# Performance work log

Hardware: AMD Instinct MI355X
Metric: run time of the kernel (lower is better)

The kernel has to match this reference:

```python
import jax, jax.numpy as jnp
import numpy as np

N_NODES = 50000
N_HYPEREDGES = 10000
N_INC = 800000  # incidences (edges in the bipartite node-hyperedge graph)
D = 128
NEG_SLOPE = 0.2


def segment_softmax(logits, seg, num_segments):
    # numerically stable softmax within segments (grouped by seg)
    m = jax.ops.segment_max(logits, seg, num_segments=num_segments)
    e = jnp.exp(logits - m[seg])
    s = jax.ops.segment_sum(e, seg, num_segments=num_segments)
    return e / s[seg]


def safe_inv(d):
    return jnp.where(d > 0, 1.0 / d, 0.0)


def setup_inputs() -> dict:
    key = jax.random.key(0)
    ks = jax.random.split(key, 8)
    x = jax.random.normal(ks[0], (N_NODES, D), dtype=jnp.float32)
    idx0 = jax.random.randint(ks[1], (N_INC,), 0, N_NODES)          # node ids
    idx1 = jax.random.randint(ks[2], (N_INC,), 0, N_HYPEREDGES)     # hyperedge ids
    hyperedge_index = jnp.stack([idx0, idx1], axis=0).astype(jnp.int64)
    hyperedge_weight = jnp.ones((N_HYPEREDGES,), dtype=jnp.float32)
    sc = 1.0 / np.sqrt(D)
    W_lin = jax.random.normal(ks[3], (D, D), dtype=jnp.float32) * sc
    W_lin2 = jax.random.normal(ks[4], (D, D), dtype=jnp.float32) * sc
    W_lin3 = jax.random.normal(ks[5], (D, D), dtype=jnp.float32) * sc
    att = jax.random.normal(ks[6], (1, 1, 2 * D), dtype=jnp.float32) * sc
    att2 = jax.random.normal(ks[7], (1, 1, 2 * D), dtype=jnp.float32) * sc
    return {"x": x, "hyperedge_index": hyperedge_index,
            "hyperedge_weight": hyperedge_weight,
            "W_lin": W_lin, "W_lin2": W_lin2, "W_lin3": W_lin3,
            "att": att, "att2": att2}


def reference(x, hyperedge_index, hyperedge_weight, W_lin, W_lin2, W_lin3, att, att2):
    N, M = N_NODES, N_HYPEREDGES
    H, F = 1, D
    idx0 = hyperedge_index[0]  # node side  [E]
    idx1 = hyperedge_index[1]  # hyperedge side [E]

    # Hyperedge(): mean-style aggregation of node features into hyperedges
    ones_e = jnp.ones_like(idx1, dtype=x.dtype)
    Binv = safe_inv(jax.ops.segment_sum(ones_e, idx1, num_segments=M))  # [M]
    he0 = jax.ops.segment_sum(x[idx0], idx1, num_segments=M) * Binv[:, None]  # [M,D]

    # linear projections
    xl = (x @ W_lin).reshape(N, H, F)      # [N,H,F]
    hl = (he0 @ W_lin2).reshape(M, H, F)   # [M,H,F]

    # first attention: node-gathered vs hyperedge-gathered, softmax grouped by node
    x_i = xl[idx0]                          # [E,H,F]
    x_j = hl[idx1]                          # [E,H,F]
    alpha = (jnp.concatenate([x_i, x_j], axis=-1) * att).sum(-1)  # [E,H]
    alpha = jax.nn.leaky_relu(alpha, NEG_SLOPE)
    alpha = segment_softmax(alpha, idx0, N)

    # degree normalizations
    Dinv = safe_inv(jax.ops.segment_sum(hyperedge_weight[idx1], idx0, num_segments=N))  # [N]

    # propagate node -> hyperedge: out_e[e] = sum Binv[e]*alpha*x[node]
    msg1 = Binv[idx1][:, None, None] * alpha[:, :, None] * x_i  # [E,H,F]
    out_e = jax.ops.segment_sum(msg1, idx1, num_segments=M)     # [M,H,F]

    # second attention with lin3-transformed hyperedge features
    he2 = (out_e.reshape(M, H * F) @ W_lin3).reshape(M, H, F)
    x_j2 = he2[idx1]
    alpha2 = (jnp.concatenate([x_i, x_j2], axis=-1) * att2).sum(-1)  # [E,H]
    alpha2 = jax.nn.leaky_relu(alpha2, NEG_SLOPE)
    alpha2 = segment_softmax(alpha2, idx0, N)

    # propagate hyperedge -> node: out_n[n] = sum Dinv[n]*alpha2*out_e[hyperedge]
    msg2 = Dinv[idx0][:, None, None] * alpha2[:, :, None] * out_e[idx1]  # [E,H,F]
    out_n = jax.ops.segment_sum(msg2, idx0, num_segments=N)              # [N,H,F]

    return out_n.reshape(N, H * F)
```

## Files before the change

kernel.cpp:

```cpp
#include <hip/hip_runtime.h>
#include <math.h>

#define DF 128
#define TILE 8192
#define CAPA 8192
#define CAPB 10240
typedef unsigned int uint;
typedef __attribute__((ext_vector_type(8))) short bf16x8;
typedef __attribute__((ext_vector_type(4))) float f32x4;

__device__ __forceinline__ float leaky(float s){ return s > 0.f ? s : 0.2f*s; }

__device__ __forceinline__ uint bfr(float f){
    uint u = __float_as_uint(f);
    return (u + 0x7fffu + ((u >> 16) & 1u)) >> 16;
}
__device__ __forceinline__ uint bf2(float a, float b){ return bfr(a) | (bfr(b) << 16); }
__device__ __forceinline__ float blo(uint v){ return __uint_as_float(v << 16); }
__device__ __forceinline__ float bhi(uint v){ return __uint_as_float(v & 0xffff0000u); }

__device__ __forceinline__ void load_edge(const void* raw, int is64, int E, int e,
                                          int& n, int& m){
    if (is64){
        const long long* p = (const long long*)raw;
        n = (int)p[e]; m = (int)p[(long long)E + e];
    } else {
        const int* p = (const int*)raw;
        n = p[e]; m = p[E + e];
    }
}

__global__ __launch_bounds__(256) void prep(
        const uint* __restrict__ raw, int* __restrict__ flag,
        int* __restrict__ gcurA, int* __restrict__ gcurB,
        const float* __restrict__ W1, const float* __restrict__ W2,
        const float* __restrict__ W3,
        const float* __restrict__ att, const float* __restrict__ att2,
        float* __restrict__ w2a, float* __restrict__ v1,
        float* __restrict__ v2, float* __restrict__ v3,
        uint* __restrict__ W1t, int E)
{
    int t = threadIdx.x;
    int bid = blockIdx.x;
    if (bid == 0){
        __shared__ int cnt;
        gcurA[t] = t*CAPA;
        gcurB[t] = t*CAPB;
        if (t == 0) cnt = 0;
        __syncthreads();
        int nz = 0;
        for (int i = 0; i < 4; i++){
            int w = 2*(t*4 + i) + 1;
            if (w < 2*E) nz += (raw[w] != 0u);
        }
        atomicAdd(&cnt, nz);
        __syncthreads();
        if (t == 0) *flag = (cnt == 0) ? 1 : 0;
    } else if (bid == 1){
        int d = t & 127;
        const float* W = (t < 128) ? W2 : W1;
        const float* a = (t < 128) ? (att + 128) : att;
        float s = 0.f;
        for (int f = 0; f < 128; f++) s += W[d*128 + f]*a[f];
        if (t < 128) w2a[d] = s; else v1[d] = s;
    } else if (bid == 2){
        __shared__ float sw3a[128];
        int d = t & 127;
        const float* W = (t < 128) ? W1 : W3;
        const float* a = (t < 128) ? att2 : (att2 + 128);
        float s = 0.f;
        for (int f = 0; f < 128; f++) s += W[d*128 + f]*a[f];
        if (t < 128) v2[d] = s; else sw3a[d] = s;
        __syncthreads();
        if (t < 128){
            float s2 = 0.f;
            for (int f = 0; f < 128; f++) s2 += W1[t*128 + f]*sw3a[f];
            v3[t] = s2;
        }
    } else {
        int base = (bid - 3)*1024;
        for (int p = base + t; p < base + 1024; p += 256){
            int f = p >> 6, dh = p & 63;
            W1t[p] = bf2(W1[(2*dh)*128 + f], W1[(2*dh + 1)*128 + f]);
        }
    }
}

__global__ __launch_bounds__(512) void bucket_scatter(const void* __restrict__ raw,
        const int* __restrict__ flag, int* __restrict__ gcurA, int* __restrict__ gcurB,
        uint* __restrict__ bktA, uint* __restrict__ bktB, int E){
    __shared__ uint stA[TILE], stB[TILE];
    __shared__ int hA[256], scA[256], cuA[256], bA[256];
    __shared__ int hB[256], scB[256], cuB[256], bB[256];
    int t = threadIdx.x;
    if (t < 256){ hA[t] = 0; hB[t] = 0; }
    __syncthreads();
    int tb = blockIdx.x*TILE;
    int cnt = min(TILE, E - tb);
    int is64 = *flag;
    for (int i = t; i < cnt; i += 512){
        int n, m; load_edge(raw, is64, E, tb + i, n, m);
        atomicAdd(&hA[n >> 8], 1);
        atomicAdd(&hB[m >> 6], 1);
    }
    __syncthreads();
    if (t < 256){ scA[t] = hA[t]; scB[t] = hB[t]; }
    __syncthreads();
    for (int off = 1; off < 256; off <<= 1){
        int vA = 0, vB = 0;
        if (t < 256 && t >= off){ vA = scA[t - off]; vB = scB[t - off]; }
        __syncthreads();
        if (t < 256){ scA[t] += vA; scB[t] += vB; }
        __syncthreads();
    }
    if (t < 256){
        scA[t] -= hA[t]; scB[t] -= hB[t];
        cuA[t] = scA[t]; cuB[t] = scB[t];
        bA[t] = atomicAdd(&gcurA[t], hA[t]);
        bB[t] = atomicAdd(&gcurB[t], hB[t]);
    }
    __syncthreads();
    for (int i = t; i < cnt; i += 512){
        int n, m; load_edge(raw, is64, E, tb + i, n, m);
        int pA = atomicAdd(&cuA[n >> 8], 1);
        stA[pA] = ((uint)n << 14) | (uint)m;
        int pB = atomicAdd(&cuB[m >> 6], 1);
        stB[pB] = ((uint)m << 16) | (uint)n;
    }
    __syncthreads();
    for (int p = t; p < cnt; p += 512){
        uint v = stA[p]; int b = (int)(v >> 22);
        bktA[bA[b] + (p - scA[b])] = v;
        uint w = stB[p]; int c = (int)(w >> 22);
        bktB[bB[c] + (p - scB[c])] = w;
    }
}

__global__ __launch_bounds__(256) void csr_edge(
        const uint* __restrict__ bktB, const int* __restrict__ gcurB,
        int* __restrict__ adj1, int2* __restrict__ rg1,
        const float* __restrict__ px, float* __restrict__ a1h, int M)
{
    __shared__ int h[64], sc[64], cu[64];
    __shared__ float fsum[64];
    int t = threadIdx.x;
    int b = blockIdx.x;
    int sb = b*CAPB;
    int total = gcurB[b] - sb;
    int kb = b << 6;
    if (t < 64){ h[t] = 0; fsum[t] = 0.f; }
    __syncthreads();
    const uint* src = bktB + sb;
    for (int i = t; i < total; i += 256)
        atomicAdd(&h[(int)(src[i] >> 16) - kb], 1);
    __syncthreads();
    if (t < 64) sc[t] = h[t];
    __syncthreads();
    for (int off = 1; off < 64; off <<= 1){
        int v = (t < 64 && t >= off) ? sc[t - off] : 0;
        __syncthreads();
        if (t < 64) sc[t] += v;
        __syncthreads();
    }
    if (t < 64){ sc[t] -= h[t]; cu[t] = sc[t]; }
    __syncthreads();
    for (int i = t; i < total; i += 256){
        uint v = src[i];
        int k = (int)(v >> 16) - kb;
        int pos = atomicAdd(&cu[k], 1);
        int n = (int)(v & 0xFFFFu);
        adj1[sb + pos] = n;
        atomicAdd(&fsum[k], px[n]);
    }
    __syncthreads();
    int key = kb + t;
    if (t < 64 && key < M){
        rg1[key] = make_int2(sb + sc[t], sb + sc[t] + h[t]);
        a1h[key] = (h[t] > 0) ? fsum[t]/(float)h[t] : 0.f;
    }
}

__global__ __launch_bounds__(256) void csr_node(
        const uint* __restrict__ bktA, const int* __restrict__ gcurA,
        int* __restrict__ adj0, int2* __restrict__ rg0,
        const float* __restrict__ a1x, const float* __restrict__ a1h,
        const float* __restrict__ hw, const float* __restrict__ pxl,
        float4* __restrict__ pk1, float* __restrict__ Dinv, int N)
{
    __shared__ int h[256], sc[256], cu[256];
    __shared__ uint sm[CAPA];
    int t = threadIdx.x;
    int b = blockIdx.x;
    int sb = b*CAPA;
    int total = gcurA[b] - sb;
    int kb = b << 8;
    h[t] = 0;
    __syncthreads();
    const uint* src = bktA + sb;
    for (int i = t; i < total; i += 256)
        atomicAdd(&h[(int)(src[i] >> 14) - kb], 1);
    __syncthreads();
    sc[t] = h[t];
    __syncthreads();
    for (int off = 1; off < 256; off <<= 1){
        int v = (t >= off) ? sc[t - off] : 0;
        __syncthreads();
        sc[t] += v;
        __syncthreads();
    }
    sc[t] -= h[t];
    cu[t] = sc[t];
    __syncthreads();
    for (int i = t; i < total; i += 256){
        uint v = src[i];
        int k = (int)(v >> 14) - kb;
        int pos = atomicAdd(&cu[k], 1);
        sm[pos] = v & 0x3FFFu;
    }
    __syncthreads();
    for (int i = t; i < total; i += 256) adj0[sb + i] = (int)sm[i];
    int key = kb + t;
    if (key < N){
        int deg = h[t], beg = sc[t];
        rg0[key] = make_int2(sb + beg, sb + beg + deg);
        float ax = a1x[key];
        float mb = -3.4e38f, wsum = 0.f;
        for (int j = 0; j < deg; j++){
            int m = (int)sm[beg + j];
            mb = fmaxf(mb, a1h[m]);
            wsum += hw[m];
        }
        float mx = leaky(ax + mb);
        float se = 0.f;
        for (int j = 0; j < deg; j++)
            se += expf(leaky(ax + a1h[(int)sm[beg + j]]) - mx);
        pk1[key] = make_float4(ax, mx, (deg > 0) ? 1.f/se : 0.f, pxl[key]);
        Dinv[key] = (wsum > 0.f) ? 1.f/wsum : 0.f;
    }
}

__global__ __launch_bounds__(256) void gemm_mfma(
    const float* __restrict__ X, const uint* __restrict__ W1t,
    const float* __restrict__ w2a, const float* __restrict__ v1,
    const float* __restrict__ v2, const float* __restrict__ v3,
    uint* __restrict__ xlb, float* __restrict__ a1x, float* __restrict__ a2x,
    float* __restrict__ px, float* __restrict__ pxl, int N)
{
    __shared__ uint4 ldsv[3072];
    char* lds = (char*)ldsv;
    int t = threadIdx.x;
    int lane = t & 63, wv = t >> 6;
    int row0 = blockIdx.x*64;

    {
        const uint4* g = (const uint4*)W1t;
        #pragma unroll
        for (int i = 0; i < 8; i++){
            int u = i*256 + t;
            int col = u >> 4;
            uint4 v = g[u];
            *(uint4*)(lds + 16384 + ((u*16) ^ ((col & 7) << 4))) = v;
        }
    }
    {
        int cg = t & 31;
        float4 c_px = ((const float4*)w2a)[cg];
        float4 c_a1 = ((const float4*)v1 )[cg];
        float4 c_a2 = ((const float4*)v2 )[cg];
        float4 c_pl = ((const float4*)v3 )[cg];
        #pragma unroll
        for (int i = 0; i < 8; i++){
            int idx = i*256 + t;
            int rl = idx >> 5;
            int row = row0 + rl;
            float4 xv = make_float4(0.f, 0.f, 0.f, 0.f);
            if (row < N) xv = ((const float4*)X)[(size_t)row*32 + cg];
            uint2 pk; pk.x = bf2(xv.x, xv.y); pk.y = bf2(xv.z, xv.w);
            *(uint2*)(lds + rl*256 + ((cg*8) ^ ((rl & 7) << 4))) = pk;
            float d0 = xv.x*c_px.x + xv.y*c_px.y + xv.z*c_px.z + xv.w*c_px.w;
            float d1 = xv.x*c_a1.x + xv.y*c_a1.y + xv.z*c_a1.z + xv.w*c_a1.w;
            float d2 = xv.x*c_a2.x + xv.y*c_a2.y + xv.z*c_a2.z + xv.w*c_a2.w;
            float d3 = xv.x*c_pl.x + xv.y*c_pl.y + xv.z*c_pl.z + xv.w*c_pl.w;
            #pragma unroll
            for (int off = 16; off > 0; off >>= 1){
                d0 += __shfl_xor(d0, off); d1 += __shfl_xor(d1, off);
                d2 += __shfl_xor(d2, off); d3 += __shfl_xor(d3, off);
            }
            if (cg == 0 && row < N){
                px[row] = d0; a1x[row] = d1; a2x[row] = d2; pxl[row] = d3;
            }
        }
    }
    __syncthreads();

    f32x4 acc[8];
    #pragma unroll
    for (int i = 0; i < 8; i++) acc[i] = (f32x4){0.f, 0.f, 0.f, 0.f};
    int arow = wv*16 + (lane & 15);
    int aswz = (arow & 7) << 4;
    int bswz = (lane & 7) << 4;
    #pragma unroll
    for (int ks = 0; ks < 4; ks++){
        int au16 = ((lane >> 4) + ks*4)*16;
        bf16x8 af = *(const bf16x8*)(lds + arow*256 + (au16 ^ aswz));
        #pragma unroll
        for (int nf = 0; nf < 8; nf++){
            int bcol = nf*16 + (lane & 15);
            bf16x8 bf = *(const bf16x8*)(lds + 16384 + bcol*256 + (au16 ^ bswz));
            acc[nf] = __builtin_amdgcn_mfma_f32_16x16x32_bf16(af, bf, acc[nf], 0, 0, 0);
        }
    }
    __syncthreads();
    #pragma unroll
    for (int nf = 0; nf < 8; nf++){
        #pragma unroll
        for (int reg = 0; reg < 4; reg++){
            int rl = wv*16 + (lane >> 4)*4 + reg;
            int col = nf*16 + (lane & 15);
            *(unsigned short*)(lds + rl*256 + ((col*2) ^ ((rl & 7) << 4))) =
                (unsigned short)bfr(acc[nf][reg]);
        }
    }
    __syncthreads();
    #pragma unroll
    for (int j = 0; j < 4; j++){
        int unit = j*64 + lane;
        int rl = wv*16 + (unit >> 4);
        int uu = unit & 15;
        uint4 v = *(const uint4*)(lds + rl*256 + ((uu*16) ^ ((rl & 7) << 4)));
        int grow = row0 + rl;
        if (grow < N) ((uint4*)xlb)[(size_t)grow*16 + uu] = v;
    }
}

__global__ __launch_bounds__(256) void agg_oute(
    const int2* __restrict__ rg1, const int* __restrict__ adj1,
    const float4* __restrict__ pk1, const float* __restrict__ a1h,
    const uint* __restrict__ xlb, uint* __restrict__ outeb,
    float* __restrict__ a2h, int M)
{
    int m = blockIdx.x*4 + (threadIdx.x >> 6);
    int lane = threadIdx.x & 63;
    if (m >= M) return;
    int2 r = rg1[m];
    int b = r.x, e = r.y, deg = e - b;
    float binv = deg > 0 ? 1.f/(float)deg : 0.f;
    float ah = a1h[m];
    int sub = lane >> 4, cg = lane & 15;
    const uint4* x4p = (const uint4*)xlb;
    float acc[8] = {0,0,0,0,0,0,0,0};
    float sca = 0.f;
    for (int base = b; base < e; base += 64){
        int cnt = min(64, e - base);
        int n = 0; float al = 0.f;
        if (lane < cnt){
            n = adj1[base + lane];
            float4 g = pk1[n];
            al = expf(leaky(g.x + ah) - g.y) * g.z;
            sca += al * g.w;
        }
        int t4 = 0;
        for (; t4 + 8 <= cnt; t4 += 8){
            int   nb0 = __shfl(n,  t4 + sub);
            float ab0 = __shfl(al, t4 + sub);
            int   nb1 = __shfl(n,  t4 + 4 + sub);
            float ab1 = __shfl(al, t4 + 4 + sub);
            uint4 v0 = x4p[(size_t)nb0*16 + cg];
            uint4 v1 = x4p[(size_t)nb1*16 + cg];
            acc[0] += ab0*blo(v0.x); acc[1] += ab0*bhi(v0.x);
            acc[2] += ab0*blo(v0.y); acc[3] += ab0*bhi(v0.y);
            acc[4] += ab0*blo(v0.z); acc[5] += ab0*bhi(v0.z);
            acc[6] += ab0*blo(v0.w); acc[7] += ab0*bhi(v0.w);
            acc[0] += ab1*blo(v1.x); acc[1] += ab1*bhi(v1.x);
            acc[2] += ab1*blo(v1.y); acc[3] += ab1*bhi(v1.y);
            acc[4] += ab1*blo(v1.z); acc[5] += ab1*bhi(v1.z);
            acc[6] += ab1*blo(v1.w); acc[7] += ab1*bhi(v1.w);
        }
        for (; t4 < cnt; t4 += 4){
            int   nb = __shfl(n,  t4 + sub);
            float ab = __shfl(al, t4 + sub);
            uint4 v = x4p[(size_t)nb*16 + cg];
            acc[0] += ab*blo(v.x); acc[1] += ab*bhi(v.x);
            acc[2] += ab*blo(v.y); acc[3] += ab*bhi(v.y);
            acc[4] += ab*blo(v.z); acc[5] += ab*bhi(v.z);
            acc[6] += ab*blo(v.w); acc[7] += ab*bhi(v.w);
        }
    }
    #pragma unroll
    for (int i = 0; i < 8; i++){
        acc[i] += __shfl_xor(acc[i], 32);
        acc[i] += __shfl_xor(acc[i], 16);
    }
    #pragma unroll
    for (int off = 32; off > 0; off >>= 1) sca += __shfl_xor(sca, off);
    if (lane < 16){
        uint4 w;
        w.x = bf2(binv*acc[0], binv*acc[1]);
        w.y = bf2(binv*acc[2], binv*acc[3]);
        w.z = bf2(binv*acc[4], binv*acc[5]);
        w.w = bf2(binv*acc[6], binv*acc[7]);
        ((uint4*)outeb)[(size_t)m*16 + cg] = w;
    }
    if (lane == 0) a2h[m] = binv*sca;
}

__global__ __launch_bounds__(256) void agg_outn(
    const int2* __restrict__ rg0, const int* __restrict__ adj0,
    const float* __restrict__ a2x, const float* __restrict__ a2h,
    const float* __restrict__ Dinv, const uint* __restrict__ outeb,
    float* __restrict__ out, int N)
{
    int n = blockIdx.x*4 + (threadIdx.x >> 6);
    int lane = threadIdx.x & 63;
    if (n >= N) return;
    int2 r = rg0[n];
    int b = r.x, e = r.y;
    float ax = a2x[n];
    float mbv = -3.4e38f;
    for (int j = b + lane; j < e; j += 64) mbv = fmaxf(mbv, a2h[adj0[j]]);
    #pragma unroll
    for (int off = 32; off > 0; off >>= 1) mbv = fmaxf(mbv, __shfl_xor(mbv, off));
    float mx = leaky(ax + mbv);
    int sub = lane >> 4, cg = lane & 15;
    const uint4* o4p = (const uint4*)outeb;
    float acc[8] = {0,0,0,0,0,0,0,0};
    float sa = 0.f;
    for (int base = b; base < e; base += 64){
        int cnt = min(64, e - base);
        int m = 0; float al = 0.f;
        if (lane < cnt){
            m = adj0[base + lane];
            al = expf(leaky(ax + a2h[m]) - mx);
            sa += al;
        }
        int t4 = 0;
        for (; t4 + 8 <= cnt; t4 += 8){
            int   mb0 = __shfl(m,  t4 + sub);
            float ab0 = __shfl(al, t4 + sub);
            int   mb1 = __shfl(m,  t4 + 4 + sub);
            float ab1 = __shfl(al, t4 + 4 + sub);
            uint4 v0 = o4p[(size_t)mb0*16 + cg];
            uint4 v1 = o4p[(size_t)mb1*16 + cg];
            acc[0] += ab0*blo(v0.x); acc[1] += ab0*bhi(v0.x);
            acc[2] += ab0*blo(v0.y); acc[3] += ab0*bhi(v0.y);
            acc[4] += ab0*blo(v0.z); acc[5] += ab0*bhi(v0.z);
            acc[6] += ab0*blo(v0.w); acc[7] += ab0*bhi(v0.w);
            acc[0] += ab1*blo(v1.x); acc[1] += ab1*bhi(v1.x);
            acc[2] += ab1*blo(v1.y); acc[3] += ab1*bhi(v1.y);
            acc[4] += ab1*blo(v1.z); acc[5] += ab1*bhi(v1.z);
            acc[6] += ab1*blo(v1.w); acc[7] += ab1*bhi(v1.w);
        }
        for (; t4 < cnt; t4 += 4){
            int   mb = __shfl(m,  t4 + sub);
            float ab = __shfl(al, t4 + sub);
            uint4 v = o4p[(size_t)mb*16 + cg];
            acc[0] += ab*blo(v.x); acc[1] += ab*bhi(v.x);
            acc[2] += ab*blo(v.y); acc[3] += ab*bhi(v.y);
            acc[4] += ab*blo(v.z); acc[5] += ab*bhi(v.z);
            acc[6] += ab*blo(v.w); acc[7] += ab*bhi(v.w);
        }
    }
    #pragma unroll
    for (int off = 32; off > 0; off >>= 1) sa += __shfl_xor(sa, off);
    #pragma unroll
    for (int i = 0; i < 8; i++){
        acc[i] += __shfl_xor(acc[i], 32);
        acc[i] += __shfl_xor(acc[i], 16);
    }
    float scale = (sa > 0.f) ? Dinv[n]/sa : 0.f;
    if (lane < 16){
        float4 o0 = make_float4(scale*acc[0], scale*acc[1], scale*acc[2], scale*acc[3]);
        float4 o1 = make_float4(scale*acc[4], scale*acc[5], scale*acc[6], scale*acc[7]);
        ((float4*)out)[(size_t)n*32 + cg*2]     = o0;
        ((float4*)out)[(size_t)n*32 + cg*2 + 1] = o1;
    }
}

extern "C" void kernel_launch(void* const* d_in, const int* in_sizes, int n_in,
                              void* d_out, int out_size, void* d_ws, size_t ws_size,
                              hipStream_t stream){
    const float* x    = (const float*)d_in[0];
    const void*  hidx = d_in[1];
    const float* hw   = (const float*)d_in[2];
    const float* W1   = (const float*)d_in[3];
    const float* W2   = (const float*)d_in[4];
    const float* W3   = (const float*)d_in[5];
    const float* att  = (const float*)d_in[6];
    const float* att2 = (const float*)d_in[7];
    float* out = (float*)d_out;

    const int N = in_sizes[0] / DF;
    const int E = in_sizes[1] / 2;
    const int M = in_sizes[2];

    char* ws = (char*)d_ws;
    size_t o = 0;
    auto take = [&](size_t bytes) -> char* {
        char* p = ws + o;
        o += (bytes + 255) & ~(size_t)255;
        return p;
    };
    const int nbA = (N + 255) >> 8;
    const int nbB = (M + 63) >> 6;

    uint*   xlb  = (uint*)  take((size_t)N*64*4);
    uint*   outeb= (uint*)  take((size_t)M*64*4);
    float*  a1x  = (float*) take((size_t)N*4);
    float*  a2x  = (float*) take((size_t)N*4);
    float*  px   = (float*) take((size_t)N*4);
    float*  pxl  = (float*) take((size_t)N*4);
    float*  Dinv = (float*) take((size_t)N*4);
    float*  a1h  = (float*) take((size_t)M*4);
    float*  a2h  = (float*) take((size_t)M*4);
    float4* pk1  = (float4*)take((size_t)N*16);
    float*  w2a  = (float*) take(DF*4);
    float*  v1   = (float*) take(DF*4);
    float*  v2   = (float*) take(DF*4);
    float*  v3   = (float*) take(DF*4);
    uint*   W1t  = (uint*)  take(128*64*4);
    int2*   rg0  = (int2*)  take((size_t)N*8);
    int2*   rg1  = (int2*)  take((size_t)M*8);
    int*    gcurA= (int*)   take(256*4);
    int*    gcurB= (int*)   take(256*4);
    uint*   bktA = (uint*)  take((size_t)nbA*CAPA*4 + TILE*4);
    uint*   bktB = (uint*)  take((size_t)nbB*CAPB*4 + TILE*4);
    int*    adj0 = (int*)   take((size_t)nbA*CAPA*4);
    int*    adj1 = (int*)   take((size_t)nbB*CAPB*4);
    int*    flag = (int*)   take(256);

    prep<<<11, 256, 0, stream>>>((const uint*)hidx, flag, gcurA, gcurB,
                                 W1, W2, W3, att, att2, w2a, v1, v2, v3, W1t, E);
    bucket_scatter<<<(E + TILE - 1)/TILE, 512, 0, stream>>>(hidx, flag,
                                 gcurA, gcurB, bktA, bktB, E);
    gemm_mfma<<<(N + 63)/64, 256, 0, stream>>>(x, W1t, w2a, v1, v2, v3,
                                               xlb, a1x, a2x, px, pxl, N);
    csr_edge<<<nbB, 256, 0, stream>>>(bktB, gcurB, adj1, rg1, px, a1h, M);
    csr_node<<<nbA, 256, 0, stream>>>(bktA, gcurA, adj0, rg0,
                                      a1x, a1h, hw, pxl, pk1, Dinv, N);
    agg_oute<<<(M + 3)/4, 256, 0, stream>>>(rg1, adj1, pk1, a1h, xlb, outeb, a2h, M);
    agg_outn<<<(N + 3)/4, 256, 0, stream>>>(rg0, adj0, a2x, a2h, Dinv, outeb, out, N);
}
```

Measured before the change: 142.1 us.

## Fuse bucket scatter with GEMM and use global max for softmax shift

Merges the edge bucket-scatter and the bf16 MFMA projection GEMM into one launch, with blocks split by block index, so the two independent stages share the machine and one launch is saved. The per-segment max pass for each softmax is replaced by a single global max of the hyperedge logit, kept in an order-preserving encoded atomicMax. That removes a full gather pass over neighbours in csr_node and agg_outn, but it changes the stabilising shift and risks underflow when logits vary widely. The agg_oute gather loop is also unrolled to keep four loads in flight.

```diff
diff --git a/kernel.cpp b/kernel.cpp
--- a/kernel.cpp
+++ b/kernel.cpp
@@ -18,6 +18,14 @@
 __device__ __forceinline__ uint bf2(float a, float b){ return bfr(a) | (bfr(b) << 16); }
 __device__ __forceinline__ float blo(uint v){ return __uint_as_float(v << 16); }
 __device__ __forceinline__ float bhi(uint v){ return __uint_as_float(v & 0xffff0000u); }
+
+__device__ __forceinline__ uint fenc(float f){
+    uint u = __float_as_uint(f);
+    return (u & 0x80000000u) ? ~u : (u | 0x80000000u);
+}
+__device__ __forceinline__ float fdec(uint k){
+    return (k & 0x80000000u) ? __uint_as_float(k ^ 0x80000000u) : __uint_as_float(~k);
+}
 
 __device__ __forceinline__ void load_edge(const void* raw, int is64, int E, int e,
                                           int& n, int& m){
@@ -31,7 +39,7 @@
 }
 
 __global__ __launch_bounds__(256) void prep(
-        const uint* __restrict__ raw, int* __restrict__ flag,
+        const uint* __restrict__ raw, int* __restrict__ ctrl,
         int* __restrict__ gcurA, int* __restrict__ gcurB,
         const float* __restrict__ W1, const float* __restrict__ W2,
         const float* __restrict__ W3,
@@ -46,7 +54,7 @@
         __shared__ int cnt;
         gcurA[t] = t*CAPA;
         gcurB[t] = t*CAPB;
-        if (t == 0) cnt = 0;
+        if (t == 0){ cnt = 0; ctrl[1] = 0; ctrl[2] = 0; }
         __syncthreads();
         int nz = 0;
         for (int i = 0; i < 4; i++){
@@ -55,7 +63,7 @@
         }
         atomicAdd(&cnt, nz);
         __syncthreads();
-        if (t == 0) *flag = (cnt == 0) ? 1 : 0;
+        if (t == 0) ctrl[0] = (cnt == 0) ? 1 : 0;
     } else if (bid == 1){
         int d = t & 127;
         const float* W = (t < 128) ? W2 : W1;
@@ -86,60 +94,158 @@
     }
 }
 
-__global__ __launch_bounds__(512) void bucket_scatter(const void* __restrict__ raw,
-        const int* __restrict__ flag, int* __restrict__ gcurA, int* __restrict__ gcurB,
-        uint* __restrict__ bktA, uint* __restrict__ bktB, int E){
-    __shared__ uint stA[TILE], stB[TILE];
-    __shared__ int hA[256], scA[256], cuA[256], bA[256];
-    __shared__ int hB[256], scB[256], cuB[256], bB[256];
+__global__ __launch_bounds__(512) void scatter_gemm(
+        const void* __restrict__ raw, const int* __restrict__ ctrl,
+        int* __restrict__ gcurA, int* __restrict__ gcurB,
+        uint* __restrict__ bktA, uint* __restrict__ bktB,
+        const float* __restrict__ X, const uint* __restrict__ W1t,
+        const float* __restrict__ w2a, const float* __restrict__ v1,
+        const float* __restrict__ v2, const float* __restrict__ v3,
+        uint* __restrict__ xlb, float* __restrict__ a1x, float* __restrict__ a2x,
+        float* __restrict__ px, float* __restrict__ pxl,
+        int E, int N, int SC)
+{
+    __shared__ char smem[73728];
     int t = threadIdx.x;
-    if (t < 256){ hA[t] = 0; hB[t] = 0; }
-    __syncthreads();
-    int tb = blockIdx.x*TILE;
-    int cnt = min(TILE, E - tb);
-    int is64 = *flag;
-    for (int i = t; i < cnt; i += 512){
-        int n, m; load_edge(raw, is64, E, tb + i, n, m);
-        atomicAdd(&hA[n >> 8], 1);
-        atomicAdd(&hB[m >> 6], 1);
-    }
-    __syncthreads();
-    if (t < 256){ scA[t] = hA[t]; scB[t] = hB[t]; }
-    __syncthreads();
-    for (int off = 1; off < 256; off <<= 1){
-        int vA = 0, vB = 0;
-        if (t < 256 && t >= off){ vA = scA[t - off]; vB = scB[t - off]; }
-        __syncthreads();
-        if (t < 256){ scA[t] += vA; scB[t] += vB; }
-        __syncthreads();
-    }
-    if (t < 256){
-        scA[t] -= hA[t]; scB[t] -= hB[t];
-        cuA[t] = scA[t]; cuB[t] = scB[t];
-        bA[t] = atomicAdd(&gcurA[t], hA[t]);
-        bB[t] = atomicAdd(&gcurB[t], hB[t]);
-    }
-    __syncthreads();
-    for (int i = t; i < cnt; i += 512){
-        int n, m; load_edge(raw, is64, E, tb + i, n, m);
-        int pA = atomicAdd(&cuA[n >> 8], 1);
-        stA[pA] = ((uint)n << 14) | (uint)m;
-        int pB = atomicAdd(&cuB[m >> 6], 1);
-        stB[pB] = ((uint)m << 16) | (uint)n;
-    }
-    __syncthreads();
-    for (int p = t; p < cnt; p += 512){
-        uint v = stA[p]; int b = (int)(v >> 22);
-        bktA[bA[b] + (p - scA[b])] = v;
-        uint w = stB[p]; int c = (int)(w >> 22);
-        bktB[bB[c] + (p - scB[c])] = w;
+    int bid = blockIdx.x;
+
+    if (bid < SC){
+        uint* stA = (uint*)smem;
+        uint* stB = (uint*)(smem + 32768);
+        int*  hA  = (int*)(smem + 65536);
+        int*  scA = hA + 256; int* cuA = hA + 512; int* bA = hA + 768;
+        int*  hB  = hA + 1024; int* scB = hA + 1280; int* cuB = hA + 1536; int* bB = hA + 1792;
+        if (t < 256){ hA[t] = 0; hB[t] = 0; }
+        __syncthreads();
+        int tb = bid*TILE;
+        int cnt = min(TILE, E - tb);
+        int is64 = ctrl[0];
+        for (int i = t; i < cnt; i += 512){
+            int n, m; load_edge(raw, is64, E, tb + i, n, m);
+            atomicAdd(&hA[n >> 8], 1);
+            atomicAdd(&hB[m >> 6], 1);
+        }
+        __syncthreads();
+        if (t < 256){ scA[t] = hA[t]; scB[t] = hB[t]; }
+        __syncthreads();
+        for (int off = 1; off < 256; off <<= 1){
+            int vA = 0, vB = 0;
+            if (t < 256 && t >= off){ vA = scA[t - off]; vB = scB[t - off]; }
+            __syncthreads();
+            if (t < 256){ scA[t] += vA; scB[t] += vB; }
+            __syncthreads();
+        }
+        if (t < 256){
+            scA[t] -= hA[t]; scB[t] -= hB[t];
+            cuA[t] = scA[t]; cuB[t] = scB[t];
+            bA[t] = atomicAdd(&gcurA[t], hA[t]);
+            bB[t] = atomicAdd(&gcurB[t], hB[t]);
+        }
+        __syncthreads();
+        for (int i = t; i < cnt; i += 512){
+            int n, m; load_edge(raw, is64, E, tb + i, n, m);
+            int pA = atomicAdd(&cuA[n >> 8], 1);
+            stA[pA] = ((uint)n << 14) | (uint)m;
+            int pB = atomicAdd(&cuB[m >> 6], 1);
+            stB[pB] = ((uint)m << 16) | (uint)n;
+        }
+        __syncthreads();
+        for (int p = t; p < cnt; p += 512){
+            uint v = stA[p]; int b = (int)(v >> 22);
+            bktA[bA[b] + (p - scA[b])] = v;
+            uint w = stB[p]; int c = (int)(w >> 22);
+            bktB[bB[c] + (p - scB[c])] = w;
+        }
+    } else {
+        char* lds = smem;
+        int lane = t & 63, wv = t >> 6;
+        int row0 = (bid - SC)*128;
+        {
+            const uint4* g = (const uint4*)W1t;
+            #pragma unroll
+            for (int i = 0; i < 4; i++){
+                int u = i*512 + t;
+                int col = u >> 4;
+                uint4 v = g[u];
+                *(uint4*)(lds + 32768 + ((u*16) ^ ((col & 7) << 4))) = v;
+            }
+        }
+        {
+            int cg = t & 31;
+            float4 c_px = ((const float4*)w2a)[cg];
+            float4 c_a1 = ((const float4*)v1 )[cg];
+            float4 c_a2 = ((const float4*)v2 )[cg];
+            float4 c_pl = ((const float4*)v3 )[cg];
+            #pragma unroll
+            for (int i = 0; i < 8; i++){
+                int idx = i*512 + t;
+                int rl = idx >> 5;
+                int row = row0 + rl;
+                float4 xv = make_float4(0.f, 0.f, 0.f, 0.f);
+                if (row < N) xv = ((const float4*)X)[(size_t)row*32 + cg];
+                uint2 pk; pk.x = bf2(xv.x, xv.y); pk.y = bf2(xv.z, xv.w);
+                *(uint2*)(lds + rl*256 + ((cg*8) ^ ((rl & 7) << 4))) = pk;
+                float d0 = xv.x*c_px.x + xv.y*c_px.y + xv.z*c_px.z + xv.w*c_px.w;
+                float d1 = xv.x*c_a1.x + xv.y*c_a1.y + xv.z*c_a1.z + xv.w*c_a1.w;
+                float d2 = xv.x*c_a2.x + xv.y*c_a2.y + xv.z*c_a2.z + xv.w*c_a2.w;
+                float d3 = xv.x*c_pl.x + xv.y*c_pl.y + xv.z*c_pl.z + xv.w*c_pl.w;
+                #pragma unroll
+                for (int off = 16; off > 0; off >>= 1){
+                    d0 += __shfl_xor(d0, off); d1 += __shfl_xor(d1, off);
+                    d2 += __shfl_xor(d2, off); d3 += __shfl_xor(d3, off);
+                }
+                if (cg == 0 && row < N){
+                    px[row] = d0; a1x[row] = d1; a2x[row] = d2; pxl[row] = d3;
+                }
+            }
+        }
+        __syncthreads();
+        f32x4 acc[8];
+        #pragma unroll
+        for (int i = 0; i < 8; i++) acc[i] = (f32x4){0.f, 0.f, 0.f, 0.f};
+        int arow = wv*16 + (lane & 15);
+        int aswz = (arow & 7) << 4;
+        int bswz = (lane & 7) << 4;
+        #pragma unroll
+        for (int ks = 0; ks < 4; ks++){
+            int au16 = ((lane >> 4) + ks*4)*16;
+            bf16x8 af = *(const bf16x8*)(lds + arow*256 + (au16 ^ aswz));
+            #pragma unroll
+            for (int nf = 0; nf < 8; nf++){
+                int bcol = nf*16 + (lane & 15);
+                bf16x8 bf = *(const bf16x8*)(lds + 32768 + bcol*256 + (au16 ^ bswz));
+                acc[nf] = __builtin_amdgcn_mfma_f32_16x16x32_bf16(af, bf, acc[nf], 0, 0, 0);
+            }
+        }
+        __syncthreads();
+        #pragma unroll
+        for (int nf = 0; nf < 8; nf++){
+            #pragma unroll
+            for (int reg = 0; reg < 4; reg++){
+                int rl = wv*16 + (lane >> 4)*4 + reg;
+                int col = nf*16 + (lane & 15);
+                *(unsigned short*)(lds + rl*256 + ((col*2) ^ ((rl & 7) << 4))) =
+                    (unsigned short)bfr(acc[nf][reg]);
+            }
+        }
+        __syncthreads();
+        #pragma unroll
+        for (int j = 0; j < 4; j++){
+            int unit = j*64 + lane;
+            int rl = wv*16 + (unit >> 4);
+            int uu = unit & 15;
+            uint4 v = *(const uint4*)(lds + rl*256 + ((uu*16) ^ ((rl & 7) << 4)));
+            int grow = row0 + rl;
+            if (grow < N) ((uint4*)xlb)[(size_t)grow*16 + uu] = v;
+        }
     }
 }
 
 __global__ __launch_bounds__(256) void csr_edge(
         const uint* __restrict__ bktB, const int* __restrict__ gcurB,
         int* __restrict__ adj1, int2* __restrict__ rg1,
-        const float* __restrict__ px, float* __restrict__ a1h, int M)
+        const float* __restrict__ px, float* __restrict__ a1h,
+        uint* __restrict__ g1key, int M)
 {
     __shared__ int h[64], sc[64], cu[64];
     __shared__ float fsum[64];
@@ -173,10 +279,18 @@
         atomicAdd(&fsum[k], px[n]);
     }
     __syncthreads();
-    int key = kb + t;
-    if (t < 64 && key < M){
-        rg1[key] = make_int2(sb + sc[t], sb + sc[t] + h[t]);
-        a1h[key] = (h[t] > 0) ? fsum[t]/(float)h[t] : 0.f;
+    if (t < 64){
+        int key = kb + t;
+        float av = -3.4e38f;
+        if (key < M){
+            av = (h[t] > 0) ? fsum[t]/(float)h[t] : 0.f;
+            rg1[key] = make_int2(sb + sc[t], sb + sc[t] + h[t]);
+            a1h[key] = av;
+        }
+        #pragma unroll
+        for (int off = 32; off > 0; off >>= 1)
+            av = fmaxf(av, __shfl_xor(av, off));
+        if (t == 0) atomicMax(g1key, fenc(av));
     }
 }
 
@@ -185,6 +299,7 @@
         int* __restrict__ adj0, int2* __restrict__ rg0,
         const float* __restrict__ a1x, const float* __restrict__ a1h,
         const float* __restrict__ hw, const float* __restrict__ pxl,
+        const uint* __restrict__ g1key,
         float4* __restrict__ pk1, float* __restrict__ Dinv, int N)
 {
     __shared__ int h[256], sc[256], cu[256];
@@ -194,6 +309,7 @@
     int sb = b*CAPA;
     int total = gcurA[b] - sb;
     int kb = b << 8;
+    float G1 = fdec(*g1key);
     h[t] = 0;
     __syncthreads();
     const uint* src = bktA + sb;
@@ -224,112 +340,15 @@
         int deg = h[t], beg = sc[t];
         rg0[key] = make_int2(sb + beg, sb + beg + deg);
         float ax = a1x[key];
-        float mb = -3.4e38f, wsum = 0.f;
+        float mx = leaky(ax + G1);
+        float se = 0.f, wsum = 0.f;
         for (int j = 0; j < deg; j++){
             int m = (int)sm[beg + j];
-            mb = fmaxf(mb, a1h[m]);
             wsum += hw[m];
-        }
-        float mx = leaky(ax + mb);
-        float se = 0.f;
-        for (int j = 0; j < deg; j++)
-            se += expf(leaky(ax + a1h[(int)sm[beg + j]]) - mx);
+            se += expf(leaky(ax + a1h[m]) - mx);
+        }
         pk1[key] = make_float4(ax, mx, (deg > 0) ? 1.f/se : 0.f, pxl[key]);
         Dinv[key] = (wsum > 0.f) ? 1.f/wsum : 0.f;
-    }
-}
-
-__global__ __launch_bounds__(256) void gemm_mfma(
-    const float* __restrict__ X, const uint* __restrict__ W1t,
-    const float* __restrict__ w2a, const float* __restrict__ v1,
-    const float* __restrict__ v2, const float* __restrict__ v3,
-    uint* __restrict__ xlb, float* __restrict__ a1x, float* __restrict__ a2x,
-    float* __restrict__ px, float* __restrict__ pxl, int N)
-{
-    __shared__ uint4 ldsv[3072];
-    char* lds = (char*)ldsv;
-    int t = threadIdx.x;
-    int lane = t & 63, wv = t >> 6;
-    int row0 = blockIdx.x*64;
-
-    {
-        const uint4* g = (const uint4*)W1t;
-        #pragma unroll
-        for (int i = 0; i < 8; i++){
-            int u = i*256 + t;
-            int col = u >> 4;
-            uint4 v = g[u];
-            *(uint4*)(lds + 16384 + ((u*16) ^ ((col & 7) << 4))) = v;
-        }
-    }
-    {
-        int cg = t & 31;
-        float4 c_px = ((const float4*)w2a)[cg];
-        float4 c_a1 = ((const float4*)v1 )[cg];
-        float4 c_a2 = ((const float4*)v2 )[cg];
-        float4 c_pl = ((const float4*)v3 )[cg];
-        #pragma unroll
-        for (int i = 0; i < 8; i++){
-            int idx = i*256 + t;
-            int rl = idx >> 5;
-            int row = row0 + rl;
-            float4 xv = make_float4(0.f, 0.f, 0.f, 0.f);
-            if (row < N) xv = ((const float4*)X)[(size_t)row*32 + cg];
-            uint2 pk; pk.x = bf2(xv.x, xv.y); pk.y = bf2(xv.z, xv.w);
-            *(uint2*)(lds + rl*256 + ((cg*8) ^ ((rl & 7) << 4))) = pk;
-            float d0 = xv.x*c_px.x + xv.y*c_px.y + xv.z*c_px.z + xv.w*c_px.w;
-            float d1 = xv.x*c_a1.x + xv.y*c_a1.y + xv.z*c_a1.z + xv.w*c_a1.w;
-            float d2 = xv.x*c_a2.x + xv.y*c_a2.y + xv.z*c_a2.z + xv.w*c_a2.w;
-            float d3 = xv.x*c_pl.x + xv.y*c_pl.y + xv.z*c_pl.z + xv.w*c_pl.w;
-            #pragma unroll
-            for (int off = 16; off > 0; off >>= 1){
-                d0 += __shfl_xor(d0, off); d1 += __shfl_xor(d1, off);
-                d2 += __shfl_xor(d2, off); d3 += __shfl_xor(d3, off);
-            }
-            if (cg == 0 && row < N){
-                px[row] = d0; a1x[row] = d1; a2x[row] = d2; pxl[row] = d3;
-            }
-        }
-    }
-    __syncthreads();
-
-    f32x4 acc[8];
-    #pragma unroll
-    for (int i = 0; i < 8; i++) acc[i] = (f32x4){0.f, 0.f, 0.f, 0.f};
-    int arow = wv*16 + (lane & 15);
-    int aswz = (arow & 7) << 4;
-    int bswz = (lane & 7) << 4;
-    #pragma unroll
-    for (int ks = 0; ks < 4; ks++){
-        int au16 = ((lane >> 4) + ks*4)*16;
-        bf16x8 af = *(const bf16x8*)(lds + arow*256 + (au16 ^ aswz));
-        #pragma unroll
-        for (int nf = 0; nf < 8; nf++){
-            int bcol = nf*16 + (lane & 15);
-            bf16x8 bf = *(const bf16x8*)(lds + 16384 + bcol*256 + (au16 ^ bswz));
-            acc[nf] = __builtin_amdgcn_mfma_f32_16x16x32_bf16(af, bf, acc[nf], 0, 0, 0);
-        }
-    }
-    __syncthreads();
-    #pragma unroll
-    for (int nf = 0; nf < 8; nf++){
-        #pragma unroll
-        for (int reg = 0; reg < 4; reg++){
-            int rl = wv*16 + (lane >> 4)*4 + reg;
-            int col = nf*16 + (lane & 15);
-            *(unsigned short*)(lds + rl*256 + ((col*2) ^ ((rl & 7) << 4))) =
-                (unsigned short)bfr(acc[nf][reg]);
-        }
-    }
-    __syncthreads();
-    #pragma unroll
-    for (int j = 0; j < 4; j++){
-        int unit = j*64 + lane;
-        int rl = wv*16 + (unit >> 4);
-        int uu = unit & 15;
-        uint4 v = *(const uint4*)(lds + rl*256 + ((uu*16) ^ ((rl & 7) << 4)));
-        int grow = row0 + rl;
-        if (grow < N) ((uint4*)xlb)[(size_t)grow*16 + uu] = v;
     }
 }
 
@@ -337,7 +356,7 @@
     const int2* __restrict__ rg1, const int* __restrict__ adj1,
     const float4* __restrict__ pk1, const float* __restrict__ a1h,
     const uint* __restrict__ xlb, uint* __restrict__ outeb,
-    float* __restrict__ a2h, int M)
+    float* __restrict__ a2h, uint* __restrict__ g2key, int M)
 {
     int m = blockIdx.x*4 + (threadIdx.x >> 6);
     int lane = threadIdx.x & 63;
@@ -360,21 +379,22 @@
             sca += al * g.w;
         }
         int t4 = 0;
-        for (; t4 + 8 <= cnt; t4 += 8){
-            int   nb0 = __shfl(n,  t4 + sub);
-            float ab0 = __shfl(al, t4 + sub);
-            int   nb1 = __shfl(n,  t4 + 4 + sub);
-            float ab1 = __shfl(al, t4 + 4 + sub);
-            uint4 v0 = x4p[(size_t)nb0*16 + cg];
-            uint4 v1 = x4p[(size_t)nb1*16 + cg];
-            acc[0] += ab0*blo(v0.x); acc[1] += ab0*bhi(v0.x);
-            acc[2] += ab0*blo(v0.y); acc[3] += ab0*bhi(v0.y);
-            acc[4] += ab0*blo(v0.z); acc[5] += ab0*bhi(v0.z);
-            acc[6] += ab0*blo(v0.w); acc[7] += ab0*bhi(v0.w);
-            acc[0] += ab1*blo(v1.x); acc[1] += ab1*bhi(v1.x);
-            acc[2] += ab1*blo(v1.y); acc[3] += ab1*bhi(v1.y);
-            acc[4] += ab1*blo(v1.z); acc[5] += ab1*bhi(v1.z);
-            acc[6] += ab1*blo(v1.w); acc[7] += ab1*bhi(v1.w);
+        for (; t4 + 16 <= cnt; t4 += 16){
+            int nb[4]; float ab[4]; uint4 v[4];
+            #pragma unroll
+            for (int k = 0; k < 4; k++){
+                nb[k] = __shfl(n,  t4 + 4*k + sub);
+                ab[k] = __shfl(al, t4 + 4*k + sub);
+            }
+            #pragma unroll
+            for (int k = 0; k < 4; k++) v[k] = x4p[(size_t)nb[k]*16 + cg];
+            #pragma unroll
+            for (int k = 0; k < 4; k++){
+                acc[0] += ab[k]*blo(v[k].x); acc[1] += ab[k]*bhi(v[k].x);
+                acc[2] += ab[k]*blo(v[k].y); acc[3] += ab[k]*bhi(v[k].y);
+                acc[4] += ab[k]*blo(v[k].z); acc[5] += ab[k]*bhi(v[k].z);
+                acc[6] += ab[k]*blo(v[k].w); acc[7] += ab[k]*bhi(v[k].w);
+            }
         }
         for (; t4 < cnt; t4 += 4){
             int   nb = __shfl(n,  t4 + sub);
@@ -401,14 +421,18 @@
         w.w = bf2(binv*acc[6], binv*acc[7]);
         ((uint4*)outeb)[(size_t)m*16 + cg] = w;
     }
-    if (lane == 0) a2h[m] = binv*sca;
+    if (lane == 0){
+        float av = binv*sca;
+        a2h[m] = av;
+        atomicMax(g2key, fenc(av));
+    }
 }
 
 __global__ __launch_bounds__(256) void agg_outn(
     const int2* __restrict__ rg0, const int* __restrict__ adj0,
     const float* __restrict__ a2x, const float* __restrict__ a2h,
     const float* __restrict__ Dinv, const uint* __restrict__ outeb,
-    float* __restrict__ out, int N)
+    const uint* __restrict__ g2key, float* __restrict__ out, int N)
 {
     int n = blockIdx.x*4 + (threadIdx.x >> 6);
     int lane = threadIdx.x & 63;
@@ -416,11 +440,7 @@
     int2 r = rg0[n];
     int b = r.x, e = r.y;
     float ax = a2x[n];
-    float mbv = -3.4e38f;
-    for (int j = b + lane; j < e; j += 64) mbv = fmaxf(mbv, a2h[adj0[j]]);
-    #pragma unroll
-    for (int off = 32; off > 0; off >>= 1) mbv = fmaxf(mbv, __shfl_xor(mbv, off));
-    float mx = leaky(ax + mbv);
+    float mx = leaky(ax + fdec(*g2key));
     int sub = lane >> 4, cg = lane & 15;
     const uint4* o4p = (const uint4*)outeb;
     float acc[8] = {0,0,0,0,0,0,0,0};
@@ -526,17 +546,23 @@
     uint*   bktB = (uint*)  take((size_t)nbB*CAPB*4 + TILE*4);
     int*    adj0 = (int*)   take((size_t)nbA*CAPA*4);
     int*    adj1 = (int*)   take((size_t)nbB*CAPB*4);
-    int*    flag = (int*)   take(256);
-
-    prep<<<11, 256, 0, stream>>>((const uint*)hidx, flag, gcurA, gcurB,
+    int*    ctrl = (int*)   take(256);
+
+    const int SC = (E + TILE - 1)/TILE;
+    const int GB = (N + 127)/128;
+
+    prep<<<11, 256, 0, stream>>>((const uint*)hidx, ctrl, gcurA, gcurB,
                                  W1, W2, W3, att, att2, w2a, v1, v2, v3, W1t, E);
-    bucket_scatter<<<(E + TILE - 1)/TILE, 512, 0, stream>>>(hidx, flag,
-                                 gcurA, gcurB, bktA, bktB, E);
-    gemm_mfma<<<(N + 63)/64, 256, 0, stream>>>(x, W1t, w2a, v1, v2, v3,
-                                               xlb, a1x, a2x, px, pxl, N);
-    csr_edge<<<nbB, 256, 0, stream>>>(bktB, gcurB, adj1, rg1, px, a1h, M);
+    scatter_gemm<<<SC + GB, 512, 0, stream>>>(hidx, ctrl, gcurA, gcurB,
+                                 bktA, bktB, x, W1t, w2a, v1, v2, v3,
+                                 xlb, a1x, a2x, px, pxl, E, N, SC);
+    csr_edge<<<nbB, 256, 0, stream>>>(bktB, gcurB, adj1, rg1, px, a1h,
+                                      (uint*)&ctrl[1], M);
     csr_node<<<nbA, 256, 0, stream>>>(bktA, gcurA, adj0, rg0,
-                                      a1x, a1h, hw, pxl, pk1, Dinv, N);
-    agg_oute<<<(M + 3)/4, 256, 0, stream>>>(rg1, adj1, pk1, a1h, xlb, outeb, a2h, M);
-    agg_outn<<<(N + 3)/4, 256, 0, stream>>>(rg0, adj0, a2x, a2h, Dinv, outeb, out, N);
-}
+                                      a1x, a1h, hw, pxl, (uint*)&ctrl[1],
+                                      pk1, Dinv, N);
+    agg_oute<<<(M + 3)/4, 256, 0, stream>>>(rg1, adj1, pk1, a1h, xlb, outeb,
+                                            a2h, (uint*)&ctrl[2], M);
+    agg_outn<<<(N + 3)/4, 256, 0, stream>>>(rg0, adj0, a2x, a2h, Dinv, outeb,
+                                            (uint*)&ctrl[2], out, N);
+}
```

After: 223.6 us. 1.57x slower.
